# Kernel optimization log

Measured on AMD Instinct MI355X. Metric: run time of the kernel, lower is better.

The kernel has to match this reference:

```python
import jax, jax.numpy as jnp
import numpy as np


def setup_inputs() -> dict:
    key = jax.random.key(0)
    k1, k2, k3 = jax.random.split(key, 3)
    # N=5 pyramid-level node features, each [B=1, C=256, H=64, W=64]
    x = jax.random.normal(k1, (5, 1, 256, 64, 64), dtype=jnp.float32)
    # Conv2d(512, 256, kernel_size=1) == per-pixel linear; stored as [in=512, out=256]
    conv_w = jax.random.normal(k2, (512, 256), dtype=jnp.float32) * 0.04
    conv_b = jax.random.normal(k3, (256,), dtype=jnp.float32) * 0.01
    return {"x": x, "conv_w": conv_w, "conv_b": conv_b}


def reference(x, conv_w, conv_b):
    # x: [N, B, C, H, W] stacked node features
    N, B, C, H, W = x.shape
    pixels = B * C * H * W
    THRESH = 0.35

    # Vectorized pairwise score (original double python loop over (i, j)):
    # make_score(x_i, x_j): target = conv1x1(cat([x_j, x_i + x_j])); |x_j - target|
    xi = x[:, None]                      # [N,1,B,C,H,W]
    xj = x[None, :]                      # [1,N,B,C,H,W]
    x_add = xi + xj                      # [N,N,B,C,H,W]
    xj_b = jnp.broadcast_to(xj, x_add.shape)
    cat = jnp.concatenate([xj_b, x_add], axis=3)          # [N,N,B,2C,H,W]
    # 1x1 conv == channel contraction
    target = jnp.einsum('ijbchw,cd->ijbdhw', cat, conv_w) \
        + conv_b[None, None, None, :, None, None]          # [N,N,B,C,H,W]
    dist = jnp.abs(xj_b - target)                          # [N,N,B,C,H,W]

    # edge_list[:, i, j] = dist(i, j) flattened over (B,C,H,W)
    edge = dist.reshape(N, N, pixels).transpose(2, 0, 1)   # [pixels, N, N]

    # node matrix: [pixels, N, 1]
    node = x.reshape(N, pixels).T[..., None]

    # F.normalize(p=2, dim=2) then keep ORIGINAL values where normalized > t
    norm = jnp.sqrt(jnp.sum(edge * edge, axis=2, keepdims=True))
    edge_n = edge / jnp.maximum(norm, 1e-12)
    edge_t = jnp.where(edge_n > THRESH, edge, jnp.zeros((), dtype=edge.dtype))

    # feat_fusion: [pixels,N,N] @ [pixels,N,1] -> [pixels,N] -> [N,pixels]
    h = (edge_t @ node)[..., 0].T                          # [N, pixels]
    out = h.reshape(N, B, C, H, W)
    return out
```

## Files before the change

### kernel.cpp

```cpp
#include <hip/hip_runtime.h>
#include <math.h>

constexpr int NIMG = 5;
constexpr int CCH  = 256;
constexpr int HWP  = 4096;
constexpr int PT   = CCH * HWP;

constexpr int BD = 64;
constexpr int BP = 64;
constexpr int BK = 32;

__device__ __forceinline__ void gload16(const float* g, float* l) {
    __builtin_amdgcn_global_load_lds(
        (const __attribute__((address_space(1))) unsigned int*)g,
        (__attribute__((address_space(3))) unsigned int*)l, 16, 0, 0);
}

__global__ __launch_bounds__(256) void uv_gemm(
    const float* __restrict__ x, const float* __restrict__ w,
    const float* __restrict__ bias, float* __restrict__ u, float* __restrict__ v)
{
    const int t  = threadIdx.x;
    const int tp = t & 15;
    const int td = t >> 4;
    const int p0 = blockIdx.x * BP;
    const int d0 = blockIdx.y * BD;
    const int n  = blockIdx.z;
    const float* xn = x + (size_t)n * PT;

    __shared__ float xs [BK][BP];
    __shared__ float w1s[BK][BD];
    __shared__ float w2s[BK][BD];

    float acc_s[4][4] = {};
    float acc_2[4][4] = {};

    const int wv = t >> 6;
    const int ln = t & 63;
    const int sr = ln >> 4;
    const int sc = (ln & 15) * 4;

    for (int c0 = 0; c0 < CCH; c0 += BK) {
        #pragma unroll
        for (int k = 0; k < 2; ++k) {
            const int r0 = (wv + k * 4) * 4;
            const int r  = r0 + sr;
            gload16(&xn[(size_t)(c0 + r) * HWP + p0 + sc], &xs[r0][0]);
            gload16(&w [(size_t)(c0 + r) * CCH + d0 + sc], &w1s[r0][0]);
            gload16(&w [(size_t)(256 + c0 + r) * CCH + d0 + sc], &w2s[r0][0]);
        }
        __syncthreads();

        #pragma unroll 8
        for (int cc = 0; cc < BK; ++cc) {
            const float4 xv  = *reinterpret_cast<const float4*>(&xs [cc][tp * 4]);
            const float4 w1v = *reinterpret_cast<const float4*>(&w1s[cc][td * 4]);
            const float4 w2v = *reinterpret_cast<const float4*>(&w2s[cc][td * 4]);
            const float xa [4] = {xv.x, xv.y, xv.z, xv.w};
            const float w2a[4] = {w2v.x, w2v.y, w2v.z, w2v.w};
            const float wsa[4] = {w1v.x + w2v.x, w1v.y + w2v.y,
                                  w1v.z + w2v.z, w1v.w + w2v.w};
            #pragma unroll
            for (int i = 0; i < 4; ++i) {
                #pragma unroll
                for (int j = 0; j < 4; ++j) {
                    acc_s[i][j] = fmaf(wsa[i], xa[j], acc_s[i][j]);
                    acc_2[i][j] = fmaf(w2a[i], xa[j], acc_2[i][j]);
                }
            }
        }
        __syncthreads();
    }

    #pragma unroll
    for (int i = 0; i < 4; ++i) {
        const int d = d0 + td * 4 + i;
        const float bd = bias[d];
        const size_t base = (size_t)d * HWP + p0 + tp * 4;
        const float4 xv = *reinterpret_cast<const float4*>(&xn[base]);
        float4 uo, vo;
        uo.x = xv.x - acc_s[i][0] - bd;
        uo.y = xv.y - acc_s[i][1] - bd;
        uo.z = xv.z - acc_s[i][2] - bd;
        uo.w = xv.w - acc_s[i][3] - bd;
        vo.x = acc_2[i][0]; vo.y = acc_2[i][1];
        vo.z = acc_2[i][2]; vo.w = acc_2[i][3];
        *reinterpret_cast<float4*>(&u[(size_t)n * PT + base]) = uo;
        *reinterpret_cast<float4*>(&v[(size_t)n * PT + base]) = vo;
    }
}

__global__ __launch_bounds__(256) void edge_out(
    const float* __restrict__ x, const float* __restrict__ u,
    const float* __restrict__ v, float* __restrict__ out)
{
    const size_t p = ((size_t)blockIdx.x * blockDim.x + threadIdx.x) * 4;
    if (p >= (size_t)PT) return;

    float xa[NIMG][4], ua[NIMG][4], va[NIMG][4];
    #pragma unroll
    for (int n2 = 0; n2 < NIMG; ++n2) {
        const float4 xv = *reinterpret_cast<const float4*>(&x[(size_t)n2 * PT + p]);
        const float4 uv = *reinterpret_cast<const float4*>(&u[(size_t)n2 * PT + p]);
        const float4 vv = *reinterpret_cast<const float4*>(&v[(size_t)n2 * PT + p]);
        xa[n2][0] = xv.x; xa[n2][1] = xv.y; xa[n2][2] = xv.z; xa[n2][3] = xv.w;
        ua[n2][0] = uv.x; ua[n2][1] = uv.y; ua[n2][2] = uv.z; ua[n2][3] = uv.w;
        va[n2][0] = vv.x; va[n2][1] = vv.y; va[n2][2] = vv.z; va[n2][3] = vv.w;
    }

    float oacc[NIMG][4];
    #pragma unroll
    for (int c = 0; c < 4; ++c) {
        #pragma unroll
        for (int i = 0; i < NIMG; ++i) {
            float e[NIMG];
            float sumsq = 0.0f;
            #pragma unroll
            for (int j = 0; j < NIMG; ++j) {
                e[j] = fabsf(ua[j][c] - va[i][c]);
                sumsq = fmaf(e[j], e[j], sumsq);
            }
            const float m = fmaxf(sqrtf(sumsq), 1e-12f);
            float h = 0.0f;
            #pragma unroll
            for (int j = 0; j < NIMG; ++j) {
                const float en = e[j] / m;
                if (en > 0.35f) h = fmaf(e[j], xa[j][c], h);
            }
            oacc[i][c] = h;
        }
    }

    #pragma unroll
    for (int i = 0; i < NIMG; ++i) {
        float4 ov = {oacc[i][0], oacc[i][1], oacc[i][2], oacc[i][3]};
        *reinterpret_cast<float4*>(&out[(size_t)i * PT + p]) = ov;
    }
}

extern "C" void kernel_launch(void* const* d_in, const int* in_sizes, int n_in,
                              void* d_out, int out_size, void* d_ws, size_t ws_size,
                              hipStream_t stream) {
    const float* x    = (const float*)d_in[0];
    const float* w    = (const float*)d_in[1];
    const float* bias = (const float*)d_in[2];
    float* out = (float*)d_out;

    float* u = (float*)d_ws;
    float* v = u + (size_t)NIMG * PT;

    dim3 g1(HWP / BP, CCH / BD, NIMG);
    uv_gemm<<<g1, 256, 0, stream>>>(x, w, bias, u, v);

    const int n4 = PT / 4;
    edge_out<<<(n4 + 255) / 256, 256, 0, stream>>>(x, u, v, out);
}
```

Before: 99.69 us.

## Fuse GEMM and edge-scoring into one kernel covering all five nodes per block

Merges the u/v GEMM and the pairwise edge/threshold kernel into a single kernel. Each block now computes the projections for all five node images over a 32-channel by 64-pixel tile and runs the edge scoring directly from registers. This removes the u/v intermediate writes and re-reads (about 40 MB of traffic) and one kernel launch. In exchange it roughly doubles per-thread accumulator registers, enlarges LDS to hold five x tiles, and halves the grid to 64x8 blocks, which may limit occupancy.

```diff
diff --git a/kernel.cpp b/kernel.cpp
--- a/kernel.cpp
+++ b/kernel.cpp
@@ -6,7 +6,7 @@
 constexpr int HWP  = 4096;
 constexpr int PT   = CCH * HWP;
 
-constexpr int BD = 64;
+constexpr int BD = 32;
 constexpr int BP = 64;
 constexpr int BK = 32;
 
@@ -16,56 +16,62 @@
         (__attribute__((address_space(3))) unsigned int*)l, 16, 0, 0);
 }
 
-__global__ __launch_bounds__(256) void uv_gemm(
+__global__ __launch_bounds__(256, 2) void fused_all(
     const float* __restrict__ x, const float* __restrict__ w,
-    const float* __restrict__ bias, float* __restrict__ u, float* __restrict__ v)
+    const float* __restrict__ bias, float* __restrict__ out)
 {
     const int t  = threadIdx.x;
     const int tp = t & 15;
     const int td = t >> 4;
     const int p0 = blockIdx.x * BP;
     const int d0 = blockIdx.y * BD;
-    const int n  = blockIdx.z;
-    const float* xn = x + (size_t)n * PT;
 
-    __shared__ float xs [BK][BP];
+    __shared__ float xs [NIMG][BK][BP];
     __shared__ float w1s[BK][BD];
     __shared__ float w2s[BK][BD];
 
-    float acc_s[4][4] = {};
-    float acc_2[4][4] = {};
+    float acc_s[NIMG][2][4] = {};
+    float acc_2[NIMG][2][4] = {};
 
-    const int wv = t >> 6;
-    const int ln = t & 63;
-    const int sr = ln >> 4;
-    const int sc = (ln & 15) * 4;
+    const int wv = t >> 6, l = t & 63;
+    const int xsr = l >> 4, xsc = (l & 15) * 4;
+    const int wsr = l >> 3, wsc = (l & 7) * 4;
 
     for (int c0 = 0; c0 < CCH; c0 += BK) {
         #pragma unroll
-        for (int k = 0; k < 2; ++k) {
-            const int r0 = (wv + k * 4) * 4;
-            const int r  = r0 + sr;
-            gload16(&xn[(size_t)(c0 + r) * HWP + p0 + sc], &xs[r0][0]);
-            gload16(&w [(size_t)(c0 + r) * CCH + d0 + sc], &w1s[r0][0]);
-            gload16(&w [(size_t)(256 + c0 + r) * CCH + d0 + sc], &w2s[r0][0]);
+        for (int n = 0; n < NIMG; ++n) {
+            #pragma unroll
+            for (int k = 0; k < 2; ++k) {
+                const int ch = wv + k * 4;
+                const int r  = ch * 4 + xsr;
+                gload16(&x[(size_t)n * PT + (size_t)(c0 + r) * HWP + p0 + xsc],
+                        &xs[n][ch * 4][0]);
+            }
+        }
+        {
+            const int r = wv * 8 + wsr;
+            gload16(&w[(size_t)(c0 + r) * CCH + d0 + wsc],       &w1s[wv * 8][0]);
+            gload16(&w[(size_t)(256 + c0 + r) * CCH + d0 + wsc], &w2s[wv * 8][0]);
         }
         __syncthreads();
 
         #pragma unroll 8
         for (int cc = 0; cc < BK; ++cc) {
-            const float4 xv  = *reinterpret_cast<const float4*>(&xs [cc][tp * 4]);
-            const float4 w1v = *reinterpret_cast<const float4*>(&w1s[cc][td * 4]);
-            const float4 w2v = *reinterpret_cast<const float4*>(&w2s[cc][td * 4]);
-            const float xa [4] = {xv.x, xv.y, xv.z, xv.w};
-            const float w2a[4] = {w2v.x, w2v.y, w2v.z, w2v.w};
-            const float wsa[4] = {w1v.x + w2v.x, w1v.y + w2v.y,
-                                  w1v.z + w2v.z, w1v.w + w2v.w};
+            const float2 w1v = *reinterpret_cast<const float2*>(&w1s[cc][td * 2]);
+            const float2 w2v = *reinterpret_cast<const float2*>(&w2s[cc][td * 2]);
+            const float w2a[2] = {w2v.x, w2v.y};
+            const float wsa[2] = {w1v.x + w2v.x, w1v.y + w2v.y};
             #pragma unroll
-            for (int i = 0; i < 4; ++i) {
+            for (int n = 0; n < NIMG; ++n) {
+                const float4 xv = *reinterpret_cast<const float4*>(&xs[n][cc][tp * 4]);
+                const float xa[4] = {xv.x, xv.y, xv.z, xv.w};
                 #pragma unroll
-                for (int j = 0; j < 4; ++j) {
-                    acc_s[i][j] = fmaf(wsa[i], xa[j], acc_s[i][j]);
-                    acc_2[i][j] = fmaf(w2a[i], xa[j], acc_2[i][j]);
+                for (int i = 0; i < 2; ++i) {
+                    #pragma unroll
+                    for (int j = 0; j < 4; ++j) {
+                        acc_s[n][i][j] = fmaf(wsa[i], xa[j], acc_s[n][i][j]);
+                        acc_2[n][i][j] = fmaf(w2a[i], xa[j], acc_2[n][i][j]);
+                    }
                 }
             }
         }
@@ -73,68 +79,48 @@
     }
 
     #pragma unroll
-    for (int i = 0; i < 4; ++i) {
-        const int d = d0 + td * 4 + i;
+    for (int r = 0; r < 2; ++r) {
+        const int d = d0 + td * 2 + r;
         const float bd = bias[d];
         const size_t base = (size_t)d * HWP + p0 + tp * 4;
-        const float4 xv = *reinterpret_cast<const float4*>(&xn[base]);
-        float4 uo, vo;
-        uo.x = xv.x - acc_s[i][0] - bd;
-        uo.y = xv.y - acc_s[i][1] - bd;
-        uo.z = xv.z - acc_s[i][2] - bd;
-        uo.w = xv.w - acc_s[i][3] - bd;
-        vo.x = acc_2[i][0]; vo.y = acc_2[i][1];
-        vo.z = acc_2[i][2]; vo.w = acc_2[i][3];
-        *reinterpret_cast<float4*>(&u[(size_t)n * PT + base]) = uo;
-        *reinterpret_cast<float4*>(&v[(size_t)n * PT + base]) = vo;
-    }
-}
 
-__global__ __launch_bounds__(256) void edge_out(
-    const float* __restrict__ x, const float* __restrict__ u,
-    const float* __restrict__ v, float* __restrict__ out)
-{
-    const size_t p = ((size_t)blockIdx.x * blockDim.x + threadIdx.x) * 4;
-    if (p >= (size_t)PT) return;
+        float xa[NIMG][4], ua[NIMG][4], va[NIMG][4];
+        #pragma unroll
+        for (int n = 0; n < NIMG; ++n) {
+            const float4 xv = *reinterpret_cast<const float4*>(&x[(size_t)n * PT + base]);
+            const float xt[4] = {xv.x, xv.y, xv.z, xv.w};
+            #pragma unroll
+            for (int q = 0; q < 4; ++q) {
+                xa[n][q] = xt[q];
+                ua[n][q] = xt[q] - acc_s[n][r][q] - bd;
+                va[n][q] = acc_2[n][r][q];
+            }
+        }
 
-    float xa[NIMG][4], ua[NIMG][4], va[NIMG][4];
-    #pragma unroll
-    for (int n2 = 0; n2 < NIMG; ++n2) {
-        const float4 xv = *reinterpret_cast<const float4*>(&x[(size_t)n2 * PT + p]);
-        const float4 uv = *reinterpret_cast<const float4*>(&u[(size_t)n2 * PT + p]);
-        const float4 vv = *reinterpret_cast<const float4*>(&v[(size_t)n2 * PT + p]);
-        xa[n2][0] = xv.x; xa[n2][1] = xv.y; xa[n2][2] = xv.z; xa[n2][3] = xv.w;
-        ua[n2][0] = uv.x; ua[n2][1] = uv.y; ua[n2][2] = uv.z; ua[n2][3] = uv.w;
-        va[n2][0] = vv.x; va[n2][1] = vv.y; va[n2][2] = vv.z; va[n2][3] = vv.w;
-    }
-
-    float oacc[NIMG][4];
-    #pragma unroll
-    for (int c = 0; c < 4; ++c) {
         #pragma unroll
         for (int i = 0; i < NIMG; ++i) {
-            float e[NIMG];
-            float sumsq = 0.0f;
+            float ho[4];
             #pragma unroll
-            for (int j = 0; j < NIMG; ++j) {
-                e[j] = fabsf(ua[j][c] - va[i][c]);
-                sumsq = fmaf(e[j], e[j], sumsq);
+            for (int q = 0; q < 4; ++q) {
+                float e[NIMG];
+                float sumsq = 0.0f;
+                #pragma unroll
+                for (int j = 0; j < NIMG; ++j) {
+                    e[j] = fabsf(ua[j][q] - va[i][q]);
+                    sumsq = fmaf(e[j], e[j], sumsq);
+                }
+                const float m = fmaxf(sqrtf(sumsq), 1e-12f);
+                float h = 0.0f;
+                #pragma unroll
+                for (int j = 0; j < NIMG; ++j) {
+                    const float en = e[j] / m;
+                    if (en > 0.35f) h = fmaf(e[j], xa[j][q], h);
+                }
+                ho[q] = h;
             }
-            const float m = fmaxf(sqrtf(sumsq), 1e-12f);
-            float h = 0.0f;
-            #pragma unroll
-            for (int j = 0; j < NIMG; ++j) {
-                const float en = e[j] / m;
-                if (en > 0.35f) h = fmaf(e[j], xa[j][c], h);
-            }
-            oacc[i][c] = h;
+            const float4 ov = {ho[0], ho[1], ho[2], ho[3]};
+            *reinterpret_cast<float4*>(&out[(size_t)i * PT + base]) = ov;
         }
-    }
-
-    #pragma unroll
-    for (int i = 0; i < NIMG; ++i) {
-        float4 ov = {oacc[i][0], oacc[i][1], oacc[i][2], oacc[i][3]};
-        *reinterpret_cast<float4*>(&out[(size_t)i * PT + p]) = ov;
     }
 }
 
@@ -146,12 +132,6 @@
     const float* bias = (const float*)d_in[2];
     float* out = (float*)d_out;
 
-    float* u = (float*)d_ws;
-    float* v = u + (size_t)NIMG * PT;
-
-    dim3 g1(HWP / BP, CCH / BD, NIMG);
-    uv_gemm<<<g1, 256, 0, stream>>>(x, w, bias, u, v);
-
-    const int n4 = PT / 4;
-    edge_out<<<(n4 + 255) / 256, 256, 0, stream>>>(x, u, v, out);
+    dim3 g(HWP / BP, CCH / BD);
+    fused_all<<<g, 256, 0, stream>>>(x, w, bias, out);
 }
```

New measurement: 87.18 us. -12.6%, faster.
